# Optimization experiments

Measured on AMD Instinct MI355X. Metric: run time of the kernel, lower is better.

## Reference

```python
import jax, jax.numpy as jnp
import numpy as np

B, D = 64, 1024
TAU = 1.0
NEG_SLOPE = 0.01  # torch LeakyReLU default


def setup_inputs() -> dict:
    key = jax.random.key(0)
    ks = jax.random.split(key, 7)
    lim = 1.0 / np.sqrt(D)
    return {
        "x": jax.random.normal(ks[0], (B, D), dtype=jnp.float32),
        "W1": jax.random.uniform(ks[1], (D, D), jnp.float32, -lim, lim),
        "b1": jax.random.uniform(ks[2], (D,), jnp.float32, -lim, lim),
        "W2": jax.random.uniform(ks[3], (D, D), jnp.float32, -lim, lim),
        "b2": jax.random.uniform(ks[4], (D,), jnp.float32, -lim, lim),
        "W3": jax.random.uniform(ks[5], (2, D), jnp.float32, -lim, lim),
        "b3": jax.random.uniform(ks[6], (2,), jnp.float32, -lim, lim),
    }


def _leaky(h):
    return jnp.where(h >= 0, h, NEG_SLOPE * h)


def _neural_sort(scores):
    # scores: [B, D]
    d = scores.shape[1]
    s = scores[..., None]                                  # [B, D, 1]
    A = jnp.abs(s - jnp.swapaxes(s, 1, 2))                 # [B, D, D] pairwise |s_i - s_j|
    # A @ (ones @ ones^T) == row-sum of A broadcast over columns
    Bsum = jnp.sum(A, axis=-1, keepdims=True)              # [B, D, 1]
    scaling = (d - 1 - 2 * jnp.arange(d)).astype(scores.dtype)  # (d+1-2*(i+1))
    C = s * scaling[None, None, :]                         # [B, D, D]
    P_max = jnp.swapaxes(C - Bsum, 1, 2)                   # [B, D, D]
    return jax.nn.softmax(P_max / TAU, axis=-1)


def reference(x, W1, b1, W2, b2, W3, b3):
    P_hat = _neural_sort(x)                                # [B, D, D]
    xs = jnp.einsum("bij,bj->bi", P_hat, x)                # soft-sorted x
    h = _leaky(xs @ W1.T + b1)
    h = _leaky(h @ W2.T + b2)
    return h @ W3.T + b3                                   # [B, 2]
```

## Files before the change

kernel.cpp:

```cpp
#include <hip/hip_runtime.h>
#include <math.h>

constexpr int Bn = 64;
constexpr int Dn = 1024;
constexpr float LOG2E = 1.4426950408889634f;
constexpr float LN2   = 0.6931471805599453f;

__device__ __forceinline__ float exp2_fast(float v) {
#if defined(__has_builtin)
#if __has_builtin(__builtin_amdgcn_exp2f)
  return __builtin_amdgcn_exp2f(v);
#else
  return exp2f(v);
#endif
#else
  return exp2f(v);
#endif
}

__global__ __launch_bounds__(256) void k_sortsoft(
    const float* __restrict__ x, float* __restrict__ xs_out,
    float* __restrict__ out) {
  __shared__ float  xs_[Dn];
  __shared__ float2 prs_[Dn];
  __shared__ int    bkt_[Dn];
  __shared__ float4 desc_[128];
  __shared__ int   cnt[64], base_[64], off_[64];
  __shared__ float Ssum[64], cN[64], cS[64];
  __shared__ float redM[4][64], redE[4][64], redD[4][64];

  int b   = blockIdx.x >> 4;
  int rc  = blockIdx.x & 15;
  int tid = threadIdx.x;

  if (tid < 64) { cnt[tid] = 0; off_[tid] = 0; Ssum[tid] = 0.f; }
  if (blockIdx.x == 0 && tid < 128) out[tid] = 0.f;
  __syncthreads();

  float4 v4 = *(const float4*)(x + b * Dn + tid * 4);
  float xv[4] = {v4.x, v4.y, v4.z, v4.w};
  int bk[4];
#pragma unroll
  for (int u = 0; u < 4; ++u) {
    float z = exp2_fast(-2.455532f * xv[u]);
    float p = 1.f / (1.f + z);
    int t = (int)(p * 64.f);
    bk[u] = t < 0 ? 0 : (t > 63 ? 63 : t);
    atomicAdd(&cnt[bk[u]], 1);
    atomicAdd(&Ssum[bk[u]], xv[u]);
  }
  __syncthreads();

  if (tid < 64) {
    int c = cnt[tid]; int si = c;
    float fs = Ssum[tid]; float ss = fs;
#pragma unroll
    for (int d = 1; d < 64; d <<= 1) {
      int oi = __shfl_up(si, d, 64);
      float os = __shfl_up(ss, d, 64);
      if (tid >= d) { si += oi; ss += os; }
    }
    base_[tid] = si - c;
    float Stot = __shfl(ss, 63, 64);
    float Slo = ss - fs;
    cN[tid] = (float)(2 * (si - c) + c - Dn);
    cS[tid] = Stot - 2.f * Slo - fs;
  }
  __syncthreads();

#pragma unroll
  for (int u = 0; u < 4; ++u) {
    int pos = base_[bk[u]] + atomicAdd(&off_[bk[u]], 1);
    xs_[pos] = xv[u];
    bkt_[pos] = bk[u];
  }
  __syncthreads();

#pragma unroll
  for (int r = 0; r < 4; ++r) {
    int p = r * 256 + tid;
    float xp = xs_[p];
    int q = bkt_[p];
    int lo = base_[q], hi = lo + cnt[q];
    float local = 0.f;
    for (int k = lo; k < hi; ++k) local += fabsf(xp - xs_[k]);
    float Bs = fmaf(xp, cN[q], cS[q]) + local;
    prs_[p] = make_float2(xp * LOG2E, -Bs * LOG2E);
  }
  __syncthreads();

  if (tid < 128) {
    int base = tid * 8;
    float xlo = xs_[base], xhi = xlo;
    int ilo = base, ihi = base;
#pragma unroll
    for (int k = 1; k < 8; ++k) {
      float xx = xs_[base + k];
      if (xx < xlo) { xlo = xx; ilo = base + k; }
      if (xx > xhi) { xhi = xx; ihi = base + k; }
    }
    float2 plo = prs_[ilo], phi = prs_[ihi];
    desc_[tid] = make_float4(plo.x, plo.y, phi.x, phi.y);
  }
  __syncthreads();

  int w = tid >> 6, lane = tid & 63;
  int i = rc * 64 + lane;
  float sc = (float)(Dn - 1 - 2 * i);
  float gm[32];
  float m = -3.4e38f;
#pragma unroll 8
  for (int q = 0; q < 32; ++q) {
    float4 d = desc_[q * 4 + w];
    float t0 = fmaf(sc, d.x, d.y);
    float t1 = fmaf(sc, d.z, d.w);
    float g = fmaxf(t0, t1);
    gm[q] = g;
    m = fmaxf(m, g);
  }
  redM[w][lane] = m;
  __syncthreads();
  float M = fmaxf(fmaxf(redM[0][lane], redM[1][lane]),
                  fmaxf(redM[2][lane], redM[3][lane]));
  float thresh = M - 32.f;

  float se = 0.f, sd = 0.f;
#pragma unroll 4
  for (int q = 0; q < 32; ++q) {
    if (__any(gm[q] > thresh)) {
      int base = (q * 4 + w) * 8;
#pragma unroll
      for (int u = 0; u < 8; ++u) {
        float2 v = prs_[base + u];
        float e = exp2_fast(fmaf(sc, v.x, v.y - M));
        se += e;
        sd = fmaf(e, v.x, sd);
      }
    }
  }
  redE[w][lane] = se;
  redD[w][lane] = sd;
  __syncthreads();
  if (tid < 64) {
    float SE = (redE[0][lane] + redE[1][lane]) + (redE[2][lane] + redE[3][lane]);
    float SD = (redD[0][lane] + redD[1][lane]) + (redD[2][lane] + redD[3][lane]);
    xs_out[b * Dn + rc * 64 + lane] = SD / SE * LN2;
  }
}

template <bool TAIL>
__global__ __launch_bounds__(256) void layer_kernel(
    const float* __restrict__ in, const float* __restrict__ W,
    const float* __restrict__ bias, float* __restrict__ out,
    const float* __restrict__ W3, const float* __restrict__ b3,
    float* __restrict__ out2) {
  __shared__ float s[8 * Dn];
  __shared__ float r2[8][8][2];
  int xcd = blockIdx.x & 7;
  int idx = blockIdx.x >> 3;
  int nc = xcd * 16 + (idx & 15);
  int bc = idx >> 4;
  int tid = threadIdx.x;
  const float* src = in + bc * 8 * Dn;
#pragma unroll
  for (int u = 0; u < 8; ++u) {
    int gl = u * 256 + tid;
    int r = gl >> 8, g = gl & 255;
    int gs = g ^ ((g >> 3) & 7);
    *(float4*)&s[r * Dn + gs * 4] = *(const float4*)(src + gl * 4);
  }
  __syncthreads();

  int c4   = tid >> 6;
  int kc   = tid & 63;
  int lane = tid & 63;
  int n0 = nc * 8 + c4 * 2;
  const float* w0 = W + (size_t)(n0 + 0) * Dn + kc * 16;
  const float* w1 = W + (size_t)(n0 + 1) * Dn + kc * 16;
  float acc0[8] = {0.f, 0.f, 0.f, 0.f, 0.f, 0.f, 0.f, 0.f};
  float acc1[8] = {0.f, 0.f, 0.f, 0.f, 0.f, 0.f, 0.f, 0.f};
#pragma unroll
  for (int j = 0; j < 4; ++j) {
    float4 wv0 = *(const float4*)(w0 + j * 4);
    float4 wv1 = *(const float4*)(w1 + j * 4);
    int g = kc * 4 + j;
    int gs = g ^ ((g >> 3) & 7);
    const float* sp = s + gs * 4;
#pragma unroll
    for (int bl = 0; bl < 8; ++bl) {
      float4 av = *(const float4*)(sp + bl * Dn);
      acc0[bl] = fmaf(av.x, wv0.x, fmaf(av.y, wv0.y,
                 fmaf(av.z, wv0.z, fmaf(av.w, wv0.w, acc0[bl]))));
      acc1[bl] = fmaf(av.x, wv1.x, fmaf(av.y, wv1.y,
                 fmaf(av.z, wv1.z, fmaf(av.w, wv1.w, acc1[bl]))));
    }
  }

  float v[16];
#pragma unroll
  for (int bl = 0; bl < 8; ++bl) { v[2 * bl] = acc0[bl]; v[2 * bl + 1] = acc1[bl]; }
#pragma unroll
  for (int bit = 0; bit < 4; ++bit) {
    int d = 1 << bit;
    bool hi = (lane & d) != 0;
#pragma unroll
    for (int i = 0; i < (8 >> bit); ++i) {
      float keep = hi ? v[2 * i + 1] : v[2 * i];
      float send = hi ? v[2 * i] : v[2 * i + 1];
      v[i] = keep + __shfl_xor(send, d, 64);
    }
  }
  float t = v[0];
  t += __shfl_xor(t, 16, 64);
  t += __shfl_xor(t, 32, 64);

  if (lane < 16) {
    int bl2 = lane >> 1, cl = lane & 1;
    int n2 = n0 + cl;
    float h = t + bias[n2];
    h = h >= 0.f ? h : 0.01f * h;
    if (!TAIL) {
      out[(bc * 8 + bl2) * Dn + n2] = h;
    } else {
      r2[bl2][c4 * 2 + cl][0] = h * W3[n2];
      r2[bl2][c4 * 2 + cl][1] = h * W3[Dn + n2];
    }
  }
  if (TAIL) {
    __syncthreads();
    if (tid < 16) {
      int bl2 = tid >> 1, o = tid & 1;
      float tt = 0.f;
#pragma unroll
      for (int q = 0; q < 8; ++q) tt += r2[bl2][q][o];
      if (nc == 0) tt += b3[o];
      atomicAdd(out2 + (bc * 8 + bl2) * 2 + o, tt);
    }
  }
}

extern "C" void kernel_launch(void* const* d_in, const int* in_sizes, int n_in,
                              void* d_out, int out_size, void* d_ws, size_t ws_size,
                              hipStream_t stream) {
  const float* x  = (const float*)d_in[0];
  const float* W1 = (const float*)d_in[1];
  const float* b1 = (const float*)d_in[2];
  const float* W2 = (const float*)d_in[3];
  const float* b2 = (const float*)d_in[4];
  const float* W3 = (const float*)d_in[5];
  const float* b3 = (const float*)d_in[6];
  float* out = (float*)d_out;
  float* ws = (float*)d_ws;

  float* xs = ws;
  float* h1 = xs + Bn * Dn;

  k_sortsoft<<<Bn * 16, 256, 0, stream>>>(x, xs, out);
  layer_kernel<false><<<1024, 256, 0, stream>>>(xs, W1, b1, h1,
                                                nullptr, nullptr, nullptr);
  layer_kernel<true><<<1024, 256, 0, stream>>>(h1, W2, b2, nullptr,
                                               W3, b3, out);
}
```

Measured before the change: 101.9 us.

## Halve sort-softmax blocks and retile GEMV layers to 4 columns per warp

The sort-softmax kernel now handles 128 rows per block instead of 64, with two warps splitting the bucket range for each row set. This halves the redundant per-block bucketing and sorting of each batch row, and the group maxima are recomputed in the second pass instead of being kept in a register array. The layer kernel now gives each warp 4 output columns over half the K range, loads W as 8 contiguous floats per lane, and combines the two K halves through shared memory. This trades extra shared-memory reduction work and higher register pressure for fewer blocks and more weight reuse per activation load.

```diff
diff --git a/kernel.cpp b/kernel.cpp
--- a/kernel.cpp
+++ b/kernel.cpp
@@ -27,10 +27,10 @@
   __shared__ float4 desc_[128];
   __shared__ int   cnt[64], base_[64], off_[64];
   __shared__ float Ssum[64], cN[64], cS[64];
-  __shared__ float redM[4][64], redE[4][64], redD[4][64];
-
-  int b   = blockIdx.x >> 4;
-  int rc  = blockIdx.x & 15;
+  __shared__ float redM[2][2][64], redE[2][2][64], redD[2][2][64];
+
+  int b   = blockIdx.x >> 3;
+  int rc2 = blockIdx.x & 7;
   int tid = threadIdx.x;
 
   if (tid < 64) { cnt[tid] = 0; off_[tid] = 0; Ssum[tid] = 0.f; }
@@ -105,30 +105,30 @@
   __syncthreads();
 
   int w = tid >> 6, lane = tid & 63;
-  int i = rc * 64 + lane;
+  int rs = w >> 1, hw = w & 1;
+  int i = rc2 * 128 + rs * 64 + lane;
   float sc = (float)(Dn - 1 - 2 * i);
-  float gm[32];
+
   float m = -3.4e38f;
 #pragma unroll 8
-  for (int q = 0; q < 32; ++q) {
-    float4 d = desc_[q * 4 + w];
+  for (int q = 0; q < 64; ++q) {
+    float4 d = desc_[2 * q + hw];
     float t0 = fmaf(sc, d.x, d.y);
     float t1 = fmaf(sc, d.z, d.w);
-    float g = fmaxf(t0, t1);
-    gm[q] = g;
-    m = fmaxf(m, g);
-  }
-  redM[w][lane] = m;
-  __syncthreads();
-  float M = fmaxf(fmaxf(redM[0][lane], redM[1][lane]),
-                  fmaxf(redM[2][lane], redM[3][lane]));
+    m = fmaxf(m, fmaxf(t0, t1));
+  }
+  redM[hw][rs][lane] = m;
+  __syncthreads();
+  float M = fmaxf(redM[0][rs][lane], redM[1][rs][lane]);
   float thresh = M - 32.f;
 
   float se = 0.f, sd = 0.f;
 #pragma unroll 4
-  for (int q = 0; q < 32; ++q) {
-    if (__any(gm[q] > thresh)) {
-      int base = (q * 4 + w) * 8;
+  for (int q = 0; q < 64; ++q) {
+    float4 d = desc_[2 * q + hw];
+    float gv = fmaxf(fmaf(sc, d.x, d.y), fmaf(sc, d.z, d.w));
+    if (__any(gv > thresh)) {
+      int base = (2 * q + hw) * 8;
 #pragma unroll
       for (int u = 0; u < 8; ++u) {
         float2 v = prs_[base + u];
@@ -138,13 +138,14 @@
       }
     }
   }
-  redE[w][lane] = se;
-  redD[w][lane] = sd;
-  __syncthreads();
-  if (tid < 64) {
-    float SE = (redE[0][lane] + redE[1][lane]) + (redE[2][lane] + redE[3][lane]);
-    float SD = (redD[0][lane] + redD[1][lane]) + (redD[2][lane] + redD[3][lane]);
-    xs_out[b * Dn + rc * 64 + lane] = SD / SE * LN2;
+  redE[hw][rs][lane] = se;
+  redD[hw][rs][lane] = sd;
+  __syncthreads();
+  if (tid < 128) {
+    int rs2 = tid >> 6, l2 = tid & 63;
+    float SE = redE[0][rs2][l2] + redE[1][rs2][l2];
+    float SD = redD[0][rs2][l2] + redD[1][rs2][l2];
+    xs_out[b * Dn + rc2 * 128 + tid] = SD / SE * LN2;
   }
 }
 
@@ -155,6 +156,7 @@
     const float* __restrict__ W3, const float* __restrict__ b3,
     float* __restrict__ out2) {
   __shared__ float s[8 * Dn];
+  __shared__ float rk[4][32];
   __shared__ float r2[8][8][2];
   int xcd = blockIdx.x & 7;
   int idx = blockIdx.x >> 3;
@@ -171,59 +173,65 @@
   }
   __syncthreads();
 
-  int c4   = tid >> 6;
-  int kc   = tid & 63;
-  int lane = tid & 63;
-  int n0 = nc * 8 + c4 * 2;
-  const float* w0 = W + (size_t)(n0 + 0) * Dn + kc * 16;
-  const float* w1 = W + (size_t)(n0 + 1) * Dn + kc * 16;
-  float acc0[8] = {0.f, 0.f, 0.f, 0.f, 0.f, 0.f, 0.f, 0.f};
-  float acc1[8] = {0.f, 0.f, 0.f, 0.f, 0.f, 0.f, 0.f, 0.f};
-#pragma unroll
-  for (int j = 0; j < 4; ++j) {
-    float4 wv0 = *(const float4*)(w0 + j * 4);
-    float4 wv1 = *(const float4*)(w1 + j * 4);
-    int g = kc * 4 + j;
+  int w = tid >> 6, lane = tid & 63;
+  int cq = w & 1, kh = w >> 1;
+  int n0 = nc * 8 + cq * 4;
+  const float* wp = W + (size_t)n0 * Dn + kh * 512 + lane * 8;
+  float acc[32];
+#pragma unroll
+  for (int i = 0; i < 32; ++i) acc[i] = 0.f;
+#pragma unroll
+  for (int j = 0; j < 2; ++j) {
+    float4 wv0 = *(const float4*)(wp + 0 * Dn + j * 4);
+    float4 wv1 = *(const float4*)(wp + 1 * Dn + j * 4);
+    float4 wv2 = *(const float4*)(wp + 2 * Dn + j * 4);
+    float4 wv3 = *(const float4*)(wp + 3 * Dn + j * 4);
+    int g = kh * 128 + lane * 2 + j;
     int gs = g ^ ((g >> 3) & 7);
     const float* sp = s + gs * 4;
 #pragma unroll
     for (int bl = 0; bl < 8; ++bl) {
       float4 av = *(const float4*)(sp + bl * Dn);
-      acc0[bl] = fmaf(av.x, wv0.x, fmaf(av.y, wv0.y,
-                 fmaf(av.z, wv0.z, fmaf(av.w, wv0.w, acc0[bl]))));
-      acc1[bl] = fmaf(av.x, wv1.x, fmaf(av.y, wv1.y,
-                 fmaf(av.z, wv1.z, fmaf(av.w, wv1.w, acc1[bl]))));
-    }
-  }
-
-  float v[16];
-#pragma unroll
-  for (int bl = 0; bl < 8; ++bl) { v[2 * bl] = acc0[bl]; v[2 * bl + 1] = acc1[bl]; }
-#pragma unroll
-  for (int bit = 0; bit < 4; ++bit) {
+      acc[bl * 4 + 0] = fmaf(av.x, wv0.x, fmaf(av.y, wv0.y,
+                        fmaf(av.z, wv0.z, fmaf(av.w, wv0.w, acc[bl * 4 + 0]))));
+      acc[bl * 4 + 1] = fmaf(av.x, wv1.x, fmaf(av.y, wv1.y,
+                        fmaf(av.z, wv1.z, fmaf(av.w, wv1.w, acc[bl * 4 + 1]))));
+      acc[bl * 4 + 2] = fmaf(av.x, wv2.x, fmaf(av.y, wv2.y,
+                        fmaf(av.z, wv2.z, fmaf(av.w, wv2.w, acc[bl * 4 + 2]))));
+      acc[bl * 4 + 3] = fmaf(av.x, wv3.x, fmaf(av.y, wv3.y,
+                        fmaf(av.z, wv3.z, fmaf(av.w, wv3.w, acc[bl * 4 + 3]))));
+    }
+  }
+
+#pragma unroll
+  for (int bit = 0; bit < 5; ++bit) {
     int d = 1 << bit;
     bool hi = (lane & d) != 0;
 #pragma unroll
-    for (int i = 0; i < (8 >> bit); ++i) {
-      float keep = hi ? v[2 * i + 1] : v[2 * i];
-      float send = hi ? v[2 * i] : v[2 * i + 1];
-      v[i] = keep + __shfl_xor(send, d, 64);
-    }
-  }
-  float t = v[0];
-  t += __shfl_xor(t, 16, 64);
+    for (int i = 0; i < (16 >> bit); ++i) {
+      float keep = hi ? acc[2 * i + 1] : acc[2 * i];
+      float send = hi ? acc[2 * i] : acc[2 * i + 1];
+      acc[i] = keep + __shfl_xor(send, d, 64);
+    }
+  }
+  float t = acc[0];
   t += __shfl_xor(t, 32, 64);
-
-  if (lane < 16) {
-    int bl2 = lane >> 1, cl = lane & 1;
-    int n2 = n0 + cl;
-    float h = t + bias[n2];
+  if (lane < 32) rk[w][lane] = t;
+  __syncthreads();
+
+  if (tid < 64) {
+    int bl2 = tid >> 3, col = tid & 7;
+    int cq2 = col >> 2, cl2 = col & 3;
+    int o = bl2 * 4 + cl2;
+    int n2 = nc * 8 + col;
+    float hs = rk[cq2][o] + rk[cq2 + 2][o];
+    float h = hs + bias[n2];
     h = h >= 0.f ? h : 0.01f * h;
     if (!TAIL) {
       out[(bc * 8 + bl2) * Dn + n2] = h;
     } else {
-      r2[bl2][c4 * 2 + cl][0] = h * W3[n2];
-      r2[bl2][c4 * 2 + cl][1] = h * W3[Dn + n2];
+      r2[bl2][col][0] = h * W3[n2];
+      r2[bl2][col][1] = h * W3[Dn + n2];
     }
   }
   if (TAIL) {
@@ -255,7 +263,7 @@
   float* xs = ws;
   float* h1 = xs + Bn * Dn;
 
-  k_sortsoft<<<Bn * 16, 256, 0, stream>>>(x, xs, out);
+  k_sortsoft<<<Bn * 8, 256, 0, stream>>>(x, xs, out);
   layer_kernel<false><<<1024, 256, 0, stream>>>(xs, W1, b1, h1,
                                                 nullptr, nullptr, nullptr);
   layer_kernel<true><<<1024, 256, 0, stream>>>(h1, W2, b2, nullptr,
```

New measurement: 103.1 us. Within noise of the previous version (+1.2%).
